# Kernel tuning notes

Measured on AMD Instinct MI355X. Metric: run time of the kernel, lower is better.

## Reference

```python
import jax, jax.numpy as jnp
import numpy as np
import math

EMBED_DIM = 256
KV_IN_DIM = 64
NUM_HEADS = 1
HEAD_DIM = EMBED_DIM // NUM_HEADS
ROPE_THETA = 10000.0


def rope_angles(end_x, end_y, dim, theta):
    # matches compute_axial_cis: axial (x,y) rotary angles, [end_x*end_y, dim//2]
    n = dim // 4
    f = 1.0 / (theta ** (np.arange(0, dim, 4)[:n].astype(np.float64) / dim))
    t = np.arange(end_x * end_y)
    tx = (t % end_x).astype(np.float64)
    ty = (t // end_x).astype(np.float64)
    ang = np.concatenate([np.outer(tx, f), np.outer(ty, f)], axis=-1)
    return (jnp.asarray(np.cos(ang), dtype=jnp.float32),
            jnp.asarray(np.sin(ang), dtype=jnp.float32))


def apply_rope(x, cos, sin):
    # x: [B,H,S,D]; cos/sin: [S,D//2]; complex rotation in real arithmetic
    xs = x.reshape(*x.shape[:-1], -1, 2)
    x0, x1 = xs[..., 0], xs[..., 1]
    o0 = x0 * cos - x1 * sin
    o1 = x0 * sin + x1 * cos
    return jnp.stack([o0, o1], axis=-1).reshape(x.shape)


def setup_inputs() -> dict:
    key = jax.random.key(0)
    ks = jax.random.split(key, 12)
    B, SQ, SK = 2, 4096, 16448
    q = jax.random.normal(ks[0], (B, SQ, EMBED_DIM), dtype=jnp.float32)
    k = jax.random.normal(ks[1], (B, SK, KV_IN_DIM), dtype=jnp.float32)
    v = jax.random.normal(ks[2], (B, SK, KV_IN_DIM), dtype=jnp.float32)
    attn_mask = jax.random.randint(ks[3], (B, SK, 1), 0, 2) > 0
    s_q = 1.0 / math.sqrt(EMBED_DIM)
    s_kv = 1.0 / math.sqrt(KV_IN_DIM)
    wq = jax.random.uniform(ks[4], (EMBED_DIM, EMBED_DIM), jnp.float32, -s_q, s_q)
    bq = jax.random.uniform(ks[5], (EMBED_DIM,), jnp.float32, -s_q, s_q)
    wk = jax.random.uniform(ks[6], (KV_IN_DIM, EMBED_DIM), jnp.float32, -s_kv, s_kv)
    bk = jax.random.uniform(ks[7], (EMBED_DIM,), jnp.float32, -s_kv, s_kv)
    wv = jax.random.uniform(ks[8], (KV_IN_DIM, EMBED_DIM), jnp.float32, -s_kv, s_kv)
    bv = jax.random.uniform(ks[9], (EMBED_DIM,), jnp.float32, -s_kv, s_kv)
    wo = jax.random.uniform(ks[10], (EMBED_DIM, EMBED_DIM), jnp.float32, -s_q, s_q)
    bo = jax.random.uniform(ks[11], (EMBED_DIM,), jnp.float32, -s_q, s_q)
    return {"q": q, "k": k, "v": v, "attn_mask": attn_mask,
            "wq": wq, "bq": bq, "wk": wk, "bk": bk, "wv": wv, "bv": bv,
            "wo": wo, "bo": bo, "num_k_exclude_rope": 64}


def reference(q, k, v, attn_mask, wq, bq, wk, bk, wv, bv, wo, bo, num_k_exclude_rope):
    B, SQ, _ = q.shape
    SK = k.shape[1]
    H, D = NUM_HEADS, HEAD_DIM
    # projections
    qh = (q @ wq + bq).reshape(B, SQ, H, D).transpose(0, 2, 1, 3)  # [B,H,SQ,D]
    kh = (k @ wk + bk).reshape(B, SK, H, D).transpose(0, 2, 1, 3)
    vh = (v @ wv + bv).reshape(B, SK, H, D).transpose(0, 2, 1, 3)
    # rotary encoding
    w = int(math.sqrt(SQ))
    cos, sin = rope_angles(w, w, D, ROPE_THETA)  # [SQ, D//2]
    qh = apply_rope(qh, cos, sin)
    num_k_rope = SK - num_k_exclude_rope
    r = num_k_rope // SQ  # rope_k_repeat: tile freqs over memory frames
    cos_k = jnp.tile(cos, (r, 1))
    sin_k = jnp.tile(sin, (r, 1))
    k_rot = apply_rope(kh[:, :, :num_k_rope], cos_k, sin_k)
    kh = jnp.concatenate([k_rot, kh[:, :, num_k_rope:]], axis=2)
    # masked SDPA; mask True = attend
    m = attn_mask[..., 0][:, None, None, :]  # [B,1,1,SK]
    scale = 1.0 / math.sqrt(D)
    scores = jnp.einsum("bhqd,bhkd->bhqk", qh, kh) * scale
    scores = jnp.where(m, scores, -jnp.inf)
    attn = jax.nn.softmax(scores, axis=-1)
    out = jnp.einsum("bhqk,bhkd->bhqd", attn, vh)
    out = out.transpose(0, 2, 1, 3).reshape(B, SQ, H * D)
    return out @ wo + bo
```

## Files before the change

### kernel.cpp

```cpp
#include <hip/hip_runtime.h>
#include <hip/hip_bf16.h>
#include <stdint.h>


typedef __attribute__((ext_vector_type(8))) short short8;
typedef __attribute__((ext_vector_type(4))) float f4;

__device__ __forceinline__ unsigned short f2bf(float x) {
  union { float f; uint32_t u; } v; v.f = x;
  return (unsigned short)((v.u + 0x7FFFu + ((v.u >> 16) & 1u)) >> 16);
}

__device__ __forceinline__ uint32_t cvtpk(float a, float b) {
  uint32_t r;
  asm("v_cvt_pk_bf16_f32 %0, %1, %2" : "=v"(r) : "v"(a), "v"(b));
  return r;
}

__device__ __forceinline__ void gl_lds16(const void* g, void* l) {
  __builtin_amdgcn_global_load_lds(
      (const __attribute__((address_space(1))) void*)g,
      (__attribute__((address_space(3))) void*)l, 16, 0, 0);
}

__global__ void rope_tab_k(float2* __restrict__ tab) {
  int idx = blockIdx.x * 256 + threadIdx.x;
  int t = idx >> 6, f = idx & 63;
  float freq = __expf(-(float)f * (9.210340371976184f / 64.0f));
  float ang = (float)t * freq;
  tab[idx] = make_float2(cosf(ang), sinf(ang));
}

__device__ __forceinline__ int mask_at(const void* mk, int f, int i) {
  if (f == 0) return ((const int*)mk)[i] != 0;
  if (f == 1) return ((const float*)mk)[i] != 0.0f;
  return ((const unsigned char*)mk)[i] != 0;
}

__global__ __launch_bounds__(256) void scan2_k(const void* __restrict__ mk,
                                               int* __restrict__ comp,
                                               int* __restrict__ ncomp) {
  __shared__ int swc[4];
  __shared__ int sflag;
  const int b = blockIdx.x, t = threadIdx.x;
  const int w4 = t >> 6, lane = t & 63;
  int okI = 1, okF = 1;
  const unsigned int* mw = (const unsigned int*)mk;
  for (int i = t; i < 2048; i += 256) {
    unsigned int x = mw[i];
    okI &= (x <= 1u);
    okF &= (x == 0u || x == 0x3F800000u);
  }
  okI = __all(okI); okF = __all(okF);
  if (t == 0) sflag = 3;
  __syncthreads();
  if (lane == 0) atomicAnd(&sflag, (okI ? 1 : 0) | (okF ? 2 : 0));
  __syncthreads();
  const int f = (sflag & 1) ? 0 : ((sflag & 2) ? 1 : 2);
  const int base = b * 16448;
  int* cb = comp + base;
  int running = 0;
  for (int it = 0; it < 65; ++it) {
    const int i = it * 256 + t;
    const int pred = (i < 16448) ? mask_at(mk, f, base + i) : 0;
    const unsigned long long bal = __ballot(pred);
    if (lane == 0) swc[w4] = __popcll(bal);
    __syncthreads();
    int wpre = 0, tot = 0;
#pragma unroll
    for (int ww = 0; ww < 4; ++ww) {
      int v = swc[ww];
      tot += v;
      if (ww < w4) wpre += v;
    }
    if (pred)
      cb[running + wpre + __popcll(bal & ((1ull << lane) - 1ull))] = i;
    running += tot;
    __syncthreads();
  }
  if (t == 0) ncomp[b] = running;
}

__global__ __launch_bounds__(256) void qproj_k(
    const float* __restrict__ q, const float* __restrict__ wq,
    const float* __restrict__ bq, const float2* __restrict__ tab,
    unsigned short* __restrict__ qh) {
  __shared__ float qs[16][256];
  const int c = threadIdx.x;
  const int rb = blockIdx.x * 16;
#pragma unroll
  for (int i = 0; i < 4; ++i) {
    const int idx = i * 256 + c;
    const int row = idx >> 6, f4i = idx & 63;
    *(float4*)&qs[row][f4i * 4] =
        *(const float4*)(q + (size_t)(rb + row) * 256 + f4i * 4);
  }
  __syncthreads();
  float acc[16];
  const float bias = bq[c];
#pragma unroll
  for (int r = 0; r < 16; ++r) acc[r] = bias;
  for (int ch = 0; ch < 4; ++ch) {
    float wreg[64];
#pragma unroll
    for (int j = 0; j < 64; ++j) wreg[j] = wq[(ch * 64 + j) * 256 + c];
#pragma unroll
    for (int r = 0; r < 16; ++r) {
      float a = acc[r];
#pragma unroll
      for (int j = 0; j < 64; j += 4) {
        const float4 x = *(const float4*)&qs[r][ch * 64 + j];
        a += x.x * wreg[j] + x.y * wreg[j + 1] + x.z * wreg[j + 2] + x.w * wreg[j + 3];
      }
      acc[r] = a;
    }
  }
  const int p = c >> 1;
#pragma unroll
  for (int r = 0; r < 16; ++r) {
    const int pos = (rb + r) & 4095;
    const float2 cs = (p < 64) ? tab[(pos & 63) * 64 + p]
                               : tab[(pos >> 6) * 64 + (p - 64)];
    const float v = acc[r];
    const float o = __shfl_xor(v, 1);
    const float res = v * cs.x + ((c & 1) ? o * cs.y : -o * cs.y);
    qh[(size_t)(rb + r) * 256 + c] = f2bf(res * 0.0625f);
  }
}

__global__ __launch_bounds__(256) void kproj_k(
    const float* __restrict__ kin, const float* __restrict__ wk,
    const float* __restrict__ bk, const float2* __restrict__ tab,
    const int* __restrict__ nker, const int* __restrict__ comp,
    const int* __restrict__ ncomp, unsigned short* __restrict__ kh) {
  __shared__ float xs[64][64];
  __shared__ int rowidx[64];
  const int c = threadIdx.x;
  const int kb = blockIdx.x, b = blockIdx.y;
  const int nc = ncomp[b];
  const int pad = (nc + 31) & ~31;
  if (kb * 64 >= pad) return;
  const int* cmp = comp + b * 16448;
  if (c < 64) rowidx[c] = (kb * 64 + c < nc) ? cmp[kb * 64 + c] : -1;
  __syncthreads();
  const float* inb = kin + (size_t)b * 16448 * 64;
#pragma unroll
  for (int i = 0; i < 4; ++i) {
    const int idx = i * 256 + c;
    const int row = idx >> 4, f4i = idx & 15;
    const int ri = rowidx[row];
    float4 v = make_float4(0.f, 0.f, 0.f, 0.f);
    if (ri >= 0) v = *(const float4*)(inb + (size_t)ri * 64 + f4i * 4);
    *(float4*)&xs[row][f4i * 4] = v;
  }
  __syncthreads();
  float wreg[64];
#pragma unroll
  for (int j = 0; j < 64; ++j) wreg[j] = wk[j * 256 + c];
  const float bias = bk[c];
  const int nrope = 16448 - nker[0];
  const int p = c >> 1;
  for (int r0 = 0; r0 < 64; r0 += 4) {
    float a0 = bias, a1 = bias, a2 = bias, a3 = bias;
#pragma unroll
    for (int j = 0; j < 64; j += 4) {
      const float4 x0 = *(const float4*)&xs[r0 + 0][j];
      const float4 x1 = *(const float4*)&xs[r0 + 1][j];
      const float4 x2 = *(const float4*)&xs[r0 + 2][j];
      const float4 x3 = *(const float4*)&xs[r0 + 3][j];
      a0 += x0.x * wreg[j] + x0.y * wreg[j + 1] + x0.z * wreg[j + 2] + x0.w * wreg[j + 3];
      a1 += x1.x * wreg[j] + x1.y * wreg[j + 1] + x1.z * wreg[j + 2] + x1.w * wreg[j + 3];
      a2 += x2.x * wreg[j] + x2.y * wreg[j + 1] + x2.z * wreg[j + 2] + x2.w * wreg[j + 3];
      a3 += x3.x * wreg[j] + x3.y * wreg[j + 1] + x3.z * wreg[j + 2] + x3.w * wreg[j + 3];
    }
    float av[4] = {a0, a1, a2, a3};
#pragma unroll
    for (int rr = 0; rr < 4; ++rr) {
      const int row = r0 + rr;
      const int ci = kb * 64 + row;
      const int oldrow = rowidx[row];
      float a = (oldrow >= 0) ? av[rr] : 0.f;
      if (oldrow >= 0 && oldrow < nrope) {
        const int pos = oldrow & 4095;
        const float2 cs = (p < 64) ? tab[(pos & 63) * 64 + p]
                                   : tab[(pos >> 6) * 64 + (p - 64)];
        const float o = __shfl_xor(a, 1);
        a = a * cs.x + ((c & 1) ? o * cs.y : -o * cs.y);
      }
      const int kk = ci & 31;
      const int rr2 = ((kk >> 2) & 1) * 16 + (kk >> 3) * 4 + (kk & 3);
      const size_t rowg = (size_t)(ci & ~31) + rr2;
      *(unsigned short*)((char*)kh + ((size_t)b * 16448 + rowg) * 512 +
                         ((2 * c) ^ ((rr2 & 7) << 4))) = f2bf(a);
    }
  }
}

__global__ __launch_bounds__(256) void vproj_k(
    const float* __restrict__ vin, const float* __restrict__ wv,
    const float* __restrict__ bv, const int* __restrict__ comp,
    const int* __restrict__ ncomp, unsigned short* __restrict__ vt) {
  __shared__ float xs[64][64];
  __shared__ int rowidx[64];
  __shared__ unsigned short vlds[64 * 258];
  const int c = threadIdx.x;
  const int kb = blockIdx.x, b = blockIdx.y;
  const int nc = ncomp[b];
  const int pad = (nc + 31) & ~31;
  if (kb * 64 >= pad) return;
  const int* cmp = comp + b * 16448;
  if (c < 64) rowidx[c] = (kb * 64 + c < nc) ? cmp[kb * 64 + c] : -1;
  __syncthreads();
  const float* inb = vin + (size_t)b * 16448 * 64;
#pragma unroll
  for (int i = 0; i < 4; ++i) {
    const int idx = i * 256 + c;
    const int row = idx >> 4, f4i = idx & 15;
    const int ri = rowidx[row];
    float4 v = make_float4(0.f, 0.f, 0.f, 0.f);
    if (ri >= 0) v = *(const float4*)(inb + (size_t)ri * 64 + f4i * 4);
    *(float4*)&xs[row][f4i * 4] = v;
  }
  __syncthreads();
  float wreg[64];
#pragma unroll
  for (int j = 0; j < 64; ++j) wreg[j] = wv[j * 256 + c];
  const float bias = bv[c];
  for (int r0 = 0; r0 < 64; r0 += 4) {
    float a0 = bias, a1 = bias, a2 = bias, a3 = bias;
#pragma unroll
    for (int j = 0; j < 64; j += 4) {
      const float4 x0 = *(const float4*)&xs[r0 + 0][j];
      const float4 x1 = *(const float4*)&xs[r0 + 1][j];
      const float4 x2 = *(const float4*)&xs[r0 + 2][j];
      const float4 x3 = *(const float4*)&xs[r0 + 3][j];
      a0 += x0.x * wreg[j] + x0.y * wreg[j + 1] + x0.z * wreg[j + 2] + x0.w * wreg[j + 3];
      a1 += x1.x * wreg[j] + x1.y * wreg[j + 1] + x1.z * wreg[j + 2] + x1.w * wreg[j + 3];
      a2 += x2.x * wreg[j] + x2.y * wreg[j + 1] + x2.z * wreg[j + 2] + x2.w * wreg[j + 3];
      a3 += x3.x * wreg[j] + x3.y * wreg[j + 1] + x3.z * wreg[j + 2] + x3.w * wreg[j + 3];
    }
    float av[4] = {a0, a1, a2, a3};
#pragma unroll
    for (int rr = 0; rr < 4; ++rr) {
      const int row = r0 + rr;
      vlds[row * 258 + c] = f2bf((rowidx[row] >= 0) ? av[rr] : 0.f);
    }
  }
  __syncthreads();
  char* tb = (char*)vt + ((size_t)b * 514 + (size_t)kb * 2) * 16384;
#pragma unroll
  for (int ti = 0; ti < 2; ++ti) {
    union { uint32_t w[16]; uint4 v4[4]; } u;
#pragma unroll
    for (int kk = 0; kk < 32; kk += 2) {
      uint32_t lo = vlds[(ti * 32 + kk) * 258 + c];
      uint32_t hi = vlds[(ti * 32 + kk + 1) * 258 + c];
      u.w[kk >> 1] = lo | (hi << 16);
    }
#pragma unroll
    for (int qd = 0; qd < 4; ++qd)
      *(uint4*)(tb + (size_t)ti * 16384 + c * 64 + qd * 16) = u.v4[qd];
  }
}

__global__ __launch_bounds__(256, 2) void attn_k(
    const unsigned short* __restrict__ qh, const unsigned short* __restrict__ kh,
    const unsigned short* __restrict__ vt, const int* __restrict__ ncomp,
    float* __restrict__ part, int nseg) {
  __shared__ __align__(16) char lds[16384];
  const int tid = threadIdx.x;
  const int w = tid >> 6, ln = tid & 63;
  const int lr = ln & 15, lg = ln >> 4;
  const int segb = blockIdx.x;
  const int qb = blockIdx.y;
  const int seg = segb >> 1, b = segb & 1;
  const int nc = ncomp[b];
  const int ntiles = (nc + 31) >> 5;
  const int t0 = seg * ntiles / nseg;
  const int t1 = (seg + 1) * ntiles / nseg;

  short8 qf[2][8];
  {
    const unsigned short* qr = qh + (size_t)(b * 4096 + qb * 128 + w * 32 + lr) * 256;
#pragma unroll
    for (int g = 0; g < 2; ++g)
#pragma unroll
      for (int kc = 0; kc < 8; ++kc)
        qf[g][kc] = *(const short8*)(qr + g * 16 * 256 + kc * 32 + lg * 8);
  }
  const f4 fz = {0.f, 0.f, 0.f, 0.f};
  f4 acc[2][16];
#pragma unroll
  for (int g = 0; g < 2; ++g)
#pragma unroll
    for (int i = 0; i < 16; ++i) acc[g][i] = fz;
  float m_[2] = {-1e30f, -1e30f}, l_[2] = {0.f, 0.f};

  const int S = (lr & 7) << 4;
  const int s6 = S & 64, Lo = (lg * 16) ^ (S & 48);
  const int baseE = lr * 512 + Lo + s6;
  const int baseO = lr * 512 + Lo + (64 - s6);

  const char* srcK = (const char*)kh + (size_t)b * 16448 * 512 + (size_t)t0 * 16384;
  const char* gV = (const char*)vt + (size_t)b * 514 * 16384 + (size_t)t0 * 16384
                   + lr * 64 + lg * 16;
  const int stoff = tid * 16;

  for (int it = t0; it < t1; ++it) {
    __syncthreads();
#pragma unroll
    for (int r = 0; r < 4; ++r)
      gl_lds16(srcK + r * 4096 + stoff, lds + r * 4096 + stoff);
    srcK += 16384;
    __syncthreads();
    f4 s[2][2] = {{fz, fz}, {fz, fz}};
#pragma unroll
    for (int kc = 0; kc < 8; ++kc) {
      const int off = ((kc & 1) ? baseO : baseE) + (kc >> 1) * 128;
      short8 k0 = *(const short8*)(lds + off);
      short8 k1 = *(const short8*)(lds + off + 8192);
      s[0][0] = __builtin_amdgcn_mfma_f32_16x16x32_bf16(k0, qf[0][kc], s[0][0], 0, 0, 0);
      s[1][0] = __builtin_amdgcn_mfma_f32_16x16x32_bf16(k0, qf[1][kc], s[1][0], 0, 0, 0);
      s[0][1] = __builtin_amdgcn_mfma_f32_16x16x32_bf16(k1, qf[0][kc], s[0][1], 0, 0, 0);
      s[1][1] = __builtin_amdgcn_mfma_f32_16x16x32_bf16(k1, qf[1][kc], s[1][1], 0, 0, 0);
    }
    if (it * 32 + 32 > nc) {
#pragma unroll
      for (int nt = 0; nt < 2; ++nt)
#pragma unroll
        for (int j = 0; j < 4; ++j)
          if (it * 32 + lg * 8 + nt * 4 + j >= nc) {
            s[0][nt][j] = -30000.f; s[1][nt][j] = -30000.f;
          }
    }
    float tm[2];
#pragma unroll
    for (int g = 0; g < 2; ++g) {
      float t = fmaxf(fmaxf(fmaxf(s[g][0][0], s[g][0][1]), fmaxf(s[g][0][2], s[g][0][3])),
                      fmaxf(fmaxf(s[g][1][0], s[g][1][1]), fmaxf(s[g][1][2], s[g][1][3])));
      t = fmaxf(t, __shfl_xor(t, 16));
      t = fmaxf(t, __shfl_xor(t, 32));
      tm[g] = t;
    }
    if (!__all(tm[0] <= m_[0] + 8.f && tm[1] <= m_[1] + 8.f)) {
#pragma unroll
      for (int g = 0; g < 2; ++g) {
        const float mn = fmaxf(m_[g], tm[g]);
        const float sc = __expf(m_[g] - mn);
        m_[g] = mn; l_[g] *= sc;
#pragma unroll
        for (int dt = 0; dt < 16; ++dt)
#pragma unroll
          for (int j = 0; j < 4; ++j) acc[g][dt][j] *= sc;
      }
    }
    short8 pf[2];
#pragma unroll
    for (int g = 0; g < 2; ++g) {
      union { uint32_t u[4]; short8 v; } pk;
      float ts = 0.f;
#pragma unroll
      for (int nt = 0; nt < 2; ++nt)
#pragma unroll
        for (int jj = 0; jj < 4; jj += 2) {
          float e0 = __expf(s[g][nt][jj] - m_[g]);
          float e1 = __expf(s[g][nt][jj + 1] - m_[g]);
          ts += e0 + e1;
          pk.u[nt * 2 + (jj >> 1)] = cvtpk(e0, e1);
        }
      ts += __shfl_xor(ts, 16);
      ts += __shfl_xor(ts, 32);
      l_[g] += ts;
      pf[g] = pk.v;
    }
#pragma unroll
    for (int bt = 0; bt < 4; ++bt) {
      short8 vf[4];
#pragma unroll
      for (int i = 0; i < 4; ++i) vf[i] = *(const short8*)(gV + (bt * 4 + i) * 1024);
#pragma unroll
      for (int dt = 0; dt < 4; ++dt) {
        acc[0][bt * 4 + dt] = __builtin_amdgcn_mfma_f32_16x16x32_bf16(vf[dt], pf[0], acc[0][bt * 4 + dt], 0, 0, 0);
        acc[1][bt * 4 + dt] = __builtin_amdgcn_mfma_f32_16x16x32_bf16(vf[dt], pf[1], acc[1][bt * 4 + dt], 0, 0, 0);
      }
    }
    gV += 16384;
  }
  const int qrow = qb * 128 + w * 32 + lr;
#pragma unroll
  for (int g = 0; g < 2; ++g) {
    float* pp = part + ((size_t)segb * 4096 + qrow + g * 16) * 260;
#pragma unroll
    for (int dt = 0; dt < 16; ++dt) *(f4*)(pp + dt * 16 + lg * 4) = acc[g][dt];
    if (lg == 0) { pp[256] = m_[g]; pp[257] = l_[g]; }
  }
}

__global__ __launch_bounds__(256) void cogemm_k(
    const float* __restrict__ part, int nseg, const float* __restrict__ wo,
    const float* __restrict__ bo, float* __restrict__ out) {
  __shared__ float rows[8][256];
  const int c = threadIdx.x;
  const int rb = blockIdx.x * 8;
  for (int r = 0; r < 8; ++r) {
    const int row = rb + r, b = row >> 12, rl = row & 4095;
    float M = -1e30f;
    for (int s = 0; s < nseg; ++s)
      M = fmaxf(M, part[(size_t)((s * 2 + b) * 4096 + rl) * 260 + 256]);
    float L = 0.f, val = 0.f;
    for (int s = 0; s < nseg; ++s) {
      size_t ix = (size_t)((s * 2 + b) * 4096 + rl) * 260;
      float wf = __expf(part[ix + 256] - M);
      L += part[ix + 257] * wf;
      val += part[ix + c] * wf;
    }
    rows[r][c] = val / L;
  }
  __syncthreads();
  float acc[8];
  const float bias = bo[c];
#pragma unroll
  for (int r = 0; r < 8; ++r) acc[r] = bias;
  for (int ch = 0; ch < 4; ++ch) {
    float wreg[64];
#pragma unroll
    for (int j = 0; j < 64; ++j) wreg[j] = wo[(ch * 64 + j) * 256 + c];
#pragma unroll
    for (int r = 0; r < 8; ++r) {
      const float* ir = &rows[r][ch * 64];
      float a = acc[r];
#pragma unroll
      for (int j = 0; j < 64; ++j) a += ir[j] * wreg[j];
      acc[r] = a;
    }
  }
#pragma unroll
  for (int r = 0; r < 8; ++r) out[(size_t)(rb + r) * 256 + c] = acc[r];
}

extern "C" void kernel_launch(void* const* d_in, const int* in_sizes, int n_in,
                              void* d_out, int out_size, void* d_ws, size_t ws_size,
                              hipStream_t stream) {
  const float* q  = (const float*)d_in[0];
  const float* k  = (const float*)d_in[1];
  const float* v  = (const float*)d_in[2];
  const void*  mk = d_in[3];
  const float* wq = (const float*)d_in[4];
  const float* bq = (const float*)d_in[5];
  const float* wk = (const float*)d_in[6];
  const float* bk = (const float*)d_in[7];
  const float* wv = (const float*)d_in[8];
  const float* bv = (const float*)d_in[9];
  const float* wo = (const float*)d_in[10];
  const float* bo = (const float*)d_in[11];
  const int* nker = (const int*)d_in[12];
  (void)in_sizes; (void)n_in; (void)out_size;

  char* ws = (char*)d_ws;
  size_t off = 0;
  auto alloc = [&](size_t sz) { size_t o = off; off = (off + sz + 255) & ~(size_t)255; return o; };
  const size_t o_tab  = alloc((size_t)64 * 64 * 8);
  const size_t o_qh   = alloc((size_t)8192 * 256 * 2);
  const size_t o_kh   = alloc((size_t)2 * 16448 * 512);
  const size_t o_vt   = alloc((size_t)2 * 514 * 16384);
  const size_t o_cmp  = alloc((size_t)2 * 16448 * 4);
  const size_t o_ncmp = alloc(256);
  const size_t o_part = off;
  auto partsz = [](int s) { return (size_t)s * 2 * 4096 * 260 * 4; };
  int nseg = 8;
  while (nseg > 1 && o_part + partsz(nseg) > ws_size) nseg >>= 1;

  float2* tab        = (float2*)(ws + o_tab);
  unsigned short* qh = (unsigned short*)(ws + o_qh);
  unsigned short* kh = (unsigned short*)(ws + o_kh);
  unsigned short* vt = (unsigned short*)(ws + o_vt);
  int* comp          = (int*)(ws + o_cmp);
  int* ncomp         = (int*)(ws + o_ncmp);
  float* part        = (float*)(ws + o_part);

  rope_tab_k<<<dim3(16), dim3(256), 0, stream>>>(tab);
  scan2_k<<<dim3(2), dim3(256), 0, stream>>>(mk, comp, ncomp);
  qproj_k<<<dim3(512), dim3(256), 0, stream>>>(q, wq, bq, tab, qh);
  kproj_k<<<dim3(257, 2), dim3(256), 0, stream>>>(k, wk, bk, tab, nker, comp, ncomp, kh);
  vproj_k<<<dim3(257, 2), dim3(256), 0, stream>>>(v, wv, bv, comp, ncomp, vt);
  attn_k<<<dim3(nseg * 2, 32), dim3(256), 0, stream>>>(qh, kh, vt, ncomp, part, nseg);
  cogemm_k<<<dim3(1024), dim3(256), 0, stream>>>(part, nseg, wo, bo, (float*)d_out);
}
```

Baseline: 441.5 us.

## Double-buffer K tiles in attention and fuse mask scan with rope table kernel

The attention kernel now double-buffers K tiles in LDS, prefetching the next tile through global_load_lds while the current one is being computed, and needs one barrier per iteration instead of two. The mask compaction scan loads all values into registers first and counts per-wave popcounts in one pass, so it no longer synchronises on every chunk. The rope table and scan kernels are merged into a single launch. Doubling LDS to 32KB could limit occupancy, and holding 65 registers per thread in the scan adds register pressure.

```diff
diff --git a/kernel.cpp b/kernel.cpp
--- a/kernel.cpp
+++ b/kernel.cpp
@@ -23,31 +23,26 @@
       (__attribute__((address_space(3))) void*)l, 16, 0, 0);
 }
 
-__global__ void rope_tab_k(float2* __restrict__ tab) {
-  int idx = blockIdx.x * 256 + threadIdx.x;
-  int t = idx >> 6, f = idx & 63;
-  float freq = __expf(-(float)f * (9.210340371976184f / 64.0f));
-  float ang = (float)t * freq;
-  tab[idx] = make_float2(cosf(ang), sinf(ang));
-}
-
-__device__ __forceinline__ int mask_at(const void* mk, int f, int i) {
-  if (f == 0) return ((const int*)mk)[i] != 0;
-  if (f == 1) return ((const float*)mk)[i] != 0.0f;
-  return ((const unsigned char*)mk)[i] != 0;
-}
-
-__global__ __launch_bounds__(256) void scan2_k(const void* __restrict__ mk,
-                                               int* __restrict__ comp,
-                                               int* __restrict__ ncomp) {
-  __shared__ int swc[4];
+__global__ __launch_bounds__(256) void scanrope_k(const void* __restrict__ mk,
+                                                  int* __restrict__ comp,
+                                                  int* __restrict__ ncomp,
+                                                  float2* __restrict__ tab) {
+  const int blk = blockIdx.x, t = threadIdx.x;
+  if (blk >= 2) {
+    const int idx = (blk - 2) * 256 + t;
+    const int tt = idx >> 6, f = idx & 63;
+    const float freq = __expf(-(float)f * (9.210340371976184f / 64.0f));
+    const float ang = (float)tt * freq;
+    tab[idx] = make_float2(cosf(ang), sinf(ang));
+    return;
+  }
+  __shared__ int cnt[4][65];
   __shared__ int sflag;
-  const int b = blockIdx.x, t = threadIdx.x;
-  const int w4 = t >> 6, lane = t & 63;
+  const int b = blk, w4 = t >> 6, lane = t & 63;
   int okI = 1, okF = 1;
   const unsigned int* mw = (const unsigned int*)mk;
   for (int i = t; i < 2048; i += 256) {
-    unsigned int x = mw[i];
+    const unsigned int x = mw[i];
     okI &= (x <= 1u);
     okF &= (x == 0u || x == 0x3F800000u);
   }
@@ -57,26 +52,34 @@
   if (lane == 0) atomicAnd(&sflag, (okI ? 1 : 0) | (okF ? 2 : 0));
   __syncthreads();
   const int f = (sflag & 1) ? 0 : ((sflag & 2) ? 1 : 2);
-  const int base = b * 16448;
-  int* cb = comp + base;
-  int running = 0;
+  const unsigned int* mwb = (const unsigned int*)mk + b * 16448;
+  const unsigned char* mbb = (const unsigned char*)mk + b * 16448;
+  uint32_t v[65];
+#pragma unroll
   for (int it = 0; it < 65; ++it) {
     const int i = it * 256 + t;
-    const int pred = (i < 16448) ? mask_at(mk, f, base + i) : 0;
-    const unsigned long long bal = __ballot(pred);
-    if (lane == 0) swc[w4] = __popcll(bal);
-    __syncthreads();
-    int wpre = 0, tot = 0;
-#pragma unroll
-    for (int ww = 0; ww < 4; ++ww) {
-      int v = swc[ww];
-      tot += v;
-      if (ww < w4) wpre += v;
-    }
-    if (pred)
-      cb[running + wpre + __popcll(bal & ((1ull << lane) - 1ull))] = i;
-    running += tot;
-    __syncthreads();
+    uint32_t x = 0;
+    if (i < 16448) x = (f < 2) ? mwb[i] : (uint32_t)mbb[i];
+    v[it] = x;
+  }
+#pragma unroll
+  for (int it = 0; it < 65; ++it) {
+    const unsigned long long bal = __ballot(v[it] != 0);
+    if (lane == 0) cnt[w4][it] = __popcll(bal);
+  }
+  __syncthreads();
+  int running = 0;
+  int* cb = comp + b * 16448;
+#pragma unroll
+  for (int it = 0; it < 65; ++it) {
+    const unsigned long long bal = __ballot(v[it] != 0);
+    int wpre = 0;
+#pragma unroll
+    for (int ww = 0; ww < 4; ++ww)
+      if (ww < w4) wpre += cnt[ww][it];
+    if (v[it] != 0)
+      cb[running + wpre + __popcll(bal & ((1ull << lane) - 1ull))] = it * 256 + t;
+    running += cnt[0][it] + cnt[1][it] + cnt[2][it] + cnt[3][it];
   }
   if (t == 0) ncomp[b] = running;
 }
@@ -267,7 +270,7 @@
     const unsigned short* __restrict__ qh, const unsigned short* __restrict__ kh,
     const unsigned short* __restrict__ vt, const int* __restrict__ ncomp,
     float* __restrict__ part, int nseg) {
-  __shared__ __align__(16) char lds[16384];
+  __shared__ __align__(16) char lds[32768];
   const int tid = threadIdx.x;
   const int w = tid >> 6, ln = tid & 63;
   const int lr = ln & 15, lg = ln >> 4;
@@ -301,24 +304,35 @@
   const int baseE = lr * 512 + Lo + s6;
   const int baseO = lr * 512 + Lo + (64 - s6);
 
-  const char* srcK = (const char*)kh + (size_t)b * 16448 * 512 + (size_t)t0 * 16384;
+  const char* khb = (const char*)kh + (size_t)b * 16448 * 512;
   const char* gV = (const char*)vt + (size_t)b * 514 * 16384 + (size_t)t0 * 16384
                    + lr * 64 + lg * 16;
+  const char* srcK = khb + (size_t)(t0 + 1) * 16384;
   const int stoff = tid * 16;
 
+  if (t0 < t1) {
+#pragma unroll
+    for (int r = 0; r < 4; ++r)
+      gl_lds16(khb + (size_t)t0 * 16384 + r * 4096 + stoff, lds + r * 4096 + stoff);
+  }
+  __syncthreads();
+
+  int cur = 0;
   for (int it = t0; it < t1; ++it) {
-    __syncthreads();
-#pragma unroll
-    for (int r = 0; r < 4; ++r)
-      gl_lds16(srcK + r * 4096 + stoff, lds + r * 4096 + stoff);
+    if (it + 1 < t1) {
+      char* dst = lds + ((cur ^ 1) << 14);
+#pragma unroll
+      for (int r = 0; r < 4; ++r)
+        gl_lds16(srcK + r * 4096 + stoff, dst + r * 4096 + stoff);
+    }
     srcK += 16384;
-    __syncthreads();
+    const char* kb_ = lds + (cur << 14);
     f4 s[2][2] = {{fz, fz}, {fz, fz}};
 #pragma unroll
     for (int kc = 0; kc < 8; ++kc) {
       const int off = ((kc & 1) ? baseO : baseE) + (kc >> 1) * 128;
-      short8 k0 = *(const short8*)(lds + off);
-      short8 k1 = *(const short8*)(lds + off + 8192);
+      short8 k0 = *(const short8*)(kb_ + off);
+      short8 k1 = *(const short8*)(kb_ + off + 8192);
       s[0][0] = __builtin_amdgcn_mfma_f32_16x16x32_bf16(k0, qf[0][kc], s[0][0], 0, 0, 0);
       s[1][0] = __builtin_amdgcn_mfma_f32_16x16x32_bf16(k0, qf[1][kc], s[1][0], 0, 0, 0);
       s[0][1] = __builtin_amdgcn_mfma_f32_16x16x32_bf16(k1, qf[0][kc], s[0][1], 0, 0, 0);
@@ -385,6 +399,8 @@
       }
     }
     gV += 16384;
+    __syncthreads();
+    cur ^= 1;
   }
   const int qrow = qb * 128 + w * 32 + lr;
 #pragma unroll
@@ -478,8 +494,7 @@
   int* ncomp         = (int*)(ws + o_ncmp);
   float* part        = (float*)(ws + o_part);
 
-  rope_tab_k<<<dim3(16), dim3(256), 0, stream>>>(tab);
-  scan2_k<<<dim3(2), dim3(256), 0, stream>>>(mk, comp, ncomp);
+  scanrope_k<<<dim3(18), dim3(256), 0, stream>>>(mk, comp, ncomp, tab);
   qproj_k<<<dim3(512), dim3(256), 0, stream>>>(q, wq, bq, tab, qh);
   kproj_k<<<dim3(257, 2), dim3(256), 0, stream>>>(k, wk, bk, tab, nker, comp, ncomp, kh);
   vproj_k<<<dim3(257, 2), dim3(256), 0, stream>>>(v, wv, bv, comp, ncomp, vt);
```

Measured after the change: 415.3 us. 1.06x faster.
